# Optimization experiments

Measured on AMD Instinct MI355X. Metric: run time of the kernel, lower is better.

## Reference

```python
import jax, jax.numpy as jnp
import numpy as np
import math

LEVEL_SHAPES = [(100, 152), (50, 76), (25, 38), (13, 19)]
BS, E, NH, NL, NP = 2, 256, 8, 4, 4


def _grid_init_bias(num_heads, num_levels, num_points):
    # faithful to MultiScaleDeformableAttention.init_weights sampling_offsets bias
    thetas = jnp.arange(num_heads, dtype=jnp.float32) * (2.0 * math.pi / num_heads)
    grid = jnp.stack([jnp.cos(thetas), jnp.sin(thetas)], -1)  # [H,2]
    grid = grid / jnp.max(jnp.abs(grid), axis=-1, keepdims=True)
    grid = jnp.tile(grid[:, None, None, :], (1, num_levels, num_points, 1))  # [H,L,P,2]
    scale = jnp.arange(1, num_points + 1, dtype=jnp.float32)[None, None, :, None]
    return (grid * scale).reshape(-1)


def setup_inputs() -> dict:
    key = jax.random.key(0)
    ks = jax.random.split(key, 10)
    nv = sum(h * w for h, w in LEVEL_SHAPES)  # 20197
    nq = nv
    query = jax.random.normal(ks[0], (BS, nq, E), dtype=jnp.float32)
    value = jax.random.normal(ks[1], (BS, nv, E), dtype=jnp.float32)
    reference_points = jax.random.uniform(ks[2], (BS, nq, NL, 2), dtype=jnp.float32)
    spatial_shapes = jnp.array(LEVEL_SHAPES, dtype=jnp.int32)
    sizes = [h * w for h, w in LEVEL_SHAPES]
    level_start_index = jnp.array(np.cumsum([0] + sizes)[:-1], dtype=jnp.int32)
    s = 1.0 / math.sqrt(E)
    # Linear params stored as [in, out]; y = x @ W + b
    Wv = jax.random.normal(ks[3], (E, E), dtype=jnp.float32) * s
    bv = jnp.zeros((E,), jnp.float32)
    Wso = jax.random.normal(ks[4], (E, NH * NL * NP * 2), dtype=jnp.float32) * 0.01
    bso = _grid_init_bias(NH, NL, NP)
    Waw = jax.random.normal(ks[5], (E, NH * NL * NP), dtype=jnp.float32) * 0.01
    baw = jnp.zeros((NH * NL * NP,), jnp.float32)
    Wo = jax.random.normal(ks[6], (E, E), dtype=jnp.float32) * s
    bo = jnp.zeros((E,), jnp.float32)
    return dict(query=query, value=value, reference_points=reference_points,
                spatial_shapes=spatial_shapes, level_start_index=level_start_index,
                Wv=Wv, bv=bv, Wso=Wso, bso=bso, Waw=Waw, baw=baw, Wo=Wo, bo=bo)


def _bilinear_sample(vl, loc, h, w):
    # vl: [bs, nh, h*w, d]; loc: [bs, nq, nh, P, 2] normalized in [0,1]
    # matches F.grid_sample(mode='bilinear', padding_mode='zeros', align_corners=False)
    bs, nh, _, d = vl.shape
    nq, P = loc.shape[1], loc.shape[3]
    x = loc[..., 0] * w - 0.5
    y = loc[..., 1] * h - 0.5
    x0 = jnp.floor(x).astype(jnp.int32); x1 = x0 + 1
    y0 = jnp.floor(y).astype(jnp.int32); y1 = y0 + 1
    wx1 = x - x0; wx0 = 1.0 - wx1
    wy1 = y - y0; wy0 = 1.0 - wy1

    def gather(ix, iy):
        valid = ((ix >= 0) & (ix < w) & (iy >= 0) & (iy < h)).astype(vl.dtype)
        idx = jnp.clip(iy, 0, h - 1) * w + jnp.clip(ix, 0, w - 1)  # [bs,nq,nh,P]
        idx = jnp.transpose(idx, (0, 2, 1, 3)).reshape(bs, nh, nq * P)
        g = jnp.take_along_axis(vl, idx[..., None], axis=2)  # [bs,nh,nq*P,d]
        g = g.reshape(bs, nh, nq, P, d).transpose(0, 2, 1, 3, 4)  # [bs,nq,nh,P,d]
        return g * valid[..., None]

    return (gather(x0, y0) * (wx0 * wy0)[..., None]
            + gather(x1, y0) * (wx1 * wy0)[..., None]
            + gather(x0, y1) * (wx0 * wy1)[..., None]
            + gather(x1, y1) * (wx1 * wy1)[..., None])


def reference(query, value, reference_points, spatial_shapes, level_start_index,
              Wv, bv, Wso, bso, Waw, baw, Wo, bo):
    bs, nq, e = query.shape
    nv = value.shape[1]
    nh, nl, npt = NH, NL, NP
    d = e // nh
    shapes = np.asarray(spatial_shapes)          # static level shapes
    starts = np.asarray(level_start_index)

    v = (value @ Wv + bv).reshape(bs, nv, nh, d).transpose(0, 2, 1, 3)  # [bs,nh,nv,d]
    so = (query @ Wso + bso).reshape(bs, nq, nh, nl, npt, 2)
    aw = jax.nn.softmax((query @ Waw + baw).reshape(bs, nq, nh, nl * npt), axis=-1)
    aw = aw.reshape(bs, nq, nh, nl, npt)

    # offset normalizer is (w, h) per level
    offset_norm = jnp.stack([spatial_shapes[:, 1], spatial_shapes[:, 0]], -1).astype(query.dtype)
    loc = reference_points[:, :, None, :, None, :] + so / offset_norm[None, None, None, :, None, :]

    out = jnp.zeros((bs, nq, nh, d), dtype=query.dtype)
    for l in range(nl):
        h, w = int(shapes[l, 0]), int(shapes[l, 1])
        s = int(starts[l])
        vl = v[:, :, s:s + h * w, :]                      # [bs,nh,h*w,d]
        sampled = _bilinear_sample(vl, loc[:, :, :, l], h, w)  # [bs,nq,nh,P,d]
        out = out + jnp.einsum('bqhpd,bqhp->bqhd', sampled, aw[:, :, :, l])

    out = out.reshape(bs, nq, e) @ Wo + bo
    return out + query  # identity residual (dropout in eval mode)
```

## Files before the change

kernel.cpp:

```cpp
#include <hip/hip_runtime.h>
#include <hip/hip_bf16.h>
#include <math.h>

constexpr int kBS = 2;
constexpr int kNQ = 20197;
constexpr int kNV = 20197;
constexpr int kM  = kBS * kNQ;
constexpr int kMT = 632;
constexpr int kMpad = kMT * 64;

__constant__ int cLH[4] = {100, 50, 25, 13};
__constant__ int cLW[4] = {152, 76, 38, 19};
__constant__ int cLS[4] = {0, 15200, 19000, 19950};

typedef __bf16 bf16x8 __attribute__((ext_vector_type(8)));
typedef float  f32x4  __attribute__((ext_vector_type(4)));

__device__ __forceinline__ unsigned short f2bf(float x) {
    unsigned u = __float_as_uint(x);
    return (unsigned short)((u + 0x7fffu + ((u >> 16) & 1u)) >> 16);
}
__device__ __forceinline__ unsigned pack2(float a, float b) {
    return (unsigned)f2bf(a) | ((unsigned)f2bf(b) << 16);
}
__device__ __forceinline__ float bflo(unsigned u) { return __uint_as_float(u << 16); }
__device__ __forceinline__ float bfhi(unsigned u) { return __uint_as_float(u & 0xffff0000u); }
__device__ __forceinline__ void gload_lds16(const void* g, void* s) {
    __builtin_amdgcn_global_load_lds(
        (const __attribute__((address_space(1))) void*)g,
        (__attribute__((address_space(3))) void*)s, 16, 0, 0);
}

__global__ __launch_bounds__(256) void prep_w(
    const float* __restrict__ Wv, const float* __restrict__ Wso,
    const float* __restrict__ Waw, const float* __restrict__ Wo,
    const float* __restrict__ bso, const float* __restrict__ baw,
    unsigned short* __restrict__ WvT, unsigned short* __restrict__ WsoawT,
    unsigned short* __restrict__ WoT, float* __restrict__ bias384)
{
    int k = blockIdx.x * 256 + threadIdx.x;
    if (k < 65536) { WvT[k] = f2bf(Wv[(k & 255) * 256 + (k >> 8)]); return; }
    k -= 65536;
    if (k < 98304) {
        int n = k >> 8, kk = k & 255;
        WsoawT[k] = f2bf(n < 256 ? Wso[kk * 256 + n] : Waw[kk * 128 + (n - 256)]);
        return;
    }
    k -= 98304;
    if (k < 65536) { WoT[k] = f2bf(Wo[(k & 255) * 256 + (k >> 8)]); return; }
    k -= 65536;
    if (k < 384) bias384[k] = (k < 256) ? bso[k] : baw[k - 256];
}

template<int AFP32, int CFP32>
__device__ __forceinline__ void gemm_core(
    const void* __restrict__ Av, const __hip_bfloat16* __restrict__ BT,
    const float* __restrict__ bias, const float* __restrict__ res,
    int N, int NT, void* __restrict__ Cv, int m0)
{
    __shared__ __hip_bfloat16 As[64 * 264];
    __shared__ __hip_bfloat16 Bs[2][128 * 32];

    const int t = threadIdx.x;
    const int wave = t >> 6, lane = t & 63;
    const int quad = lane >> 4, l16 = lane & 15;
    const int mw = (wave & 1) * 32, nw = (wave >> 1) * 64;

    auto issueB = [&](int nti, int kc, int buf) {
        #pragma unroll
        for (int j = 0; j < 2; ++j) {
            int off = j * 4096 + t * 16;
            int row = off >> 6, kb = off & 63;
            gload_lds16((const char*)BT + (size_t)(nti * 128 + row) * 512 + kc * 64 + kb,
                        (char*)&Bs[buf][0] + off);
        }
    };

    issueB(0, 0, 0);

    if (AFP32) {
        const float* af = (const float*)Av;
        #pragma unroll
        for (int p = 0; p < 16; ++p) {
            int idx = p * 256 + t;
            int row = idx >> 6, col4 = idx & 63;
            float4 f = make_float4(0.f, 0.f, 0.f, 0.f);
            if (m0 + row < kM)
                f = *(const float4*)(af + (size_t)(m0 + row) * 256 + col4 * 4);
            uint2 u = make_uint2(pack2(f.x, f.y), pack2(f.z, f.w));
            *(uint2*)(void*)&As[row * 264 + col4 * 4] = u;
        }
    } else {
        const unsigned short* ab = (const unsigned short*)Av;
        #pragma unroll
        for (int p = 0; p < 8; ++p) {
            int idx = p * 256 + t;
            int row = idx >> 5, ch = idx & 31;
            uint4 u = *(const uint4*)(ab + (size_t)(m0 + row) * 256 + ch * 8);
            *(uint4*)(void*)&As[row * 264 + ch * 8] = u;
        }
    }

    for (int nti = 0; nti < NT; ++nti) {
        f32x4 acc[2][4] = {};
        for (int kc = 0; kc < 8; ++kc) {
            __syncthreads();
            if (kc < 7)             issueB(nti, kc + 1, (kc + 1) & 1);
            else if (nti + 1 < NT)  issueB(nti + 1, 0, 0);
            bf16x8 afr[2], bfr[4];
            #pragma unroll
            for (int mt = 0; mt < 2; ++mt)
                afr[mt] = *(const bf16x8*)(const void*)
                    &As[(mw + mt * 16 + l16) * 264 + kc * 32 + quad * 8];
            #pragma unroll
            for (int nt = 0; nt < 4; ++nt)
                bfr[nt] = *(const bf16x8*)(const void*)
                    &Bs[kc & 1][(nw + nt * 16 + l16) * 32 + quad * 8];
            #pragma unroll
            for (int mt = 0; mt < 2; ++mt)
                #pragma unroll
                for (int nt = 0; nt < 4; ++nt)
                    acc[mt][nt] = __builtin_amdgcn_mfma_f32_16x16x32_bf16(
                        afr[mt], bfr[nt], acc[mt][nt], 0, 0, 0);
        }
        const int n0g = nti * 128;
        #pragma unroll
        for (int nt = 0; nt < 4; ++nt) {
            int col = n0g + nw + nt * 16 + l16;
            float bvv = bias[col];
            #pragma unroll
            for (int mt = 0; mt < 2; ++mt) {
                #pragma unroll
                for (int i = 0; i < 4; ++i) {
                    int row = m0 + mw + mt * 16 + quad * 4 + i;
                    if (row < kM) {
                        float val = acc[mt][nt][i] + bvv;
                        if (CFP32)
                            ((float*)Cv)[(size_t)row * N + col] =
                                val + res[(size_t)row * N + col];
                        else
                            ((unsigned short*)Cv)[(size_t)row * N + col] = f2bf(val);
                    }
                }
            }
        }
    }
}

__global__ __launch_bounds__(256, 3) void gemm_dual(
    const float* __restrict__ value, const __hip_bfloat16* __restrict__ WvT,
    const float* __restrict__ bv, unsigned short* __restrict__ v_b,
    const float* __restrict__ query, const __hip_bfloat16* __restrict__ WsoawT,
    const float* __restrict__ b384, unsigned short* __restrict__ soaw)
{
    const int m0 = blockIdx.y * 64;
    const float* A; const __hip_bfloat16* BT; const float* bias;
    unsigned short* C; int N, NT;
    if (blockIdx.x == 0) { A = value; BT = WvT;    bias = bv;   C = v_b;  N = 256; NT = 2; }
    else                 { A = query; BT = WsoawT; bias = b384; C = soaw; N = 384; NT = 3; }
    gemm_core<1, 0>(A, BT, bias, nullptr, N, NT, C, m0);
}

__global__ __launch_bounds__(256, 3) void gemm_final(
    const unsigned short* __restrict__ mid_b, const __hip_bfloat16* __restrict__ WoT,
    const float* __restrict__ bo, const float* __restrict__ query,
    float* __restrict__ out)
{
    gemm_core<0, 1>(mid_b, WoT, bo, query, 256, 2, out, blockIdx.y * 64);
}

__global__ __launch_bounds__(128) void msda_sample(
    const __hip_bfloat16* __restrict__ v,
    const __hip_bfloat16* __restrict__ soaw,
    const float* __restrict__ rp,
    __hip_bfloat16* __restrict__ mid)
{
    const int bq = blockIdx.x;
    const int b  = bq >= kNQ;
    const int t  = threadIdx.x;

    __shared__ int   sOff[128 * 5];
    __shared__ float sW[128 * 5];

    {
        const int h = t >> 4, lp = t & 15, l = lp >> 2;
        unsigned sopk = *(const unsigned*)(const void*)(soaw + (size_t)bq * 384 + 2 * t);
        float logit = bflo((unsigned)*(const unsigned short*)(const void*)
                           (soaw + (size_t)bq * 384 + 256 + t));
        float2 rr = *(const float2*)(rp + (size_t)bq * 8 + l * 2);
        float sx = bflo(sopk), sy = bfhi(sopk);

        float mx = logit;
        #pragma unroll
        for (int s = 8; s >= 1; s >>= 1) mx = fmaxf(mx, __shfl_xor(mx, s, 16));
        float e = __expf(logit - mx);
        float sum = e;
        #pragma unroll
        for (int s = 8; s >= 1; s >>= 1) sum += __shfl_xor(sum, s, 16);
        float w = e / sum;

        const int ww = cLW[l], hh = cLH[l];
        const float fw = (float)ww, fh = (float)hh;
        float x = rr.x * fw + sx - 0.5f;
        float y = rr.y * fh + sy - 0.5f;
        float xf = floorf(x), yf = floorf(y);
        int x0 = (int)xf, y0 = (int)yf;
        float wx1 = x - xf, wx0 = 1.f - wx1;
        float wy1 = y - yf, wy0 = 1.f - wy1;
        bool vx0 = (x0 >= 0) & (x0 < ww);
        bool vx1 = (x0 >= -1) & (x0 + 1 < ww);
        bool vy0 = (y0 >= 0) & (y0 < hh);
        bool vy1 = (y0 >= -1) & (y0 + 1 < hh);
        int cx0 = min(max(x0, 0), ww - 1);
        int cx1 = min(max(x0 + 1, 0), ww - 1);
        int cy0 = min(max(y0, 0), hh - 1);
        int cy1 = min(max(y0 + 1, 0), hh - 1);
        const int base = cLS[l] * 256 + h * 32;
        sOff[t * 5 + 0] = base + (cy0 * ww + cx0) * 256;
        sOff[t * 5 + 1] = base + (cy0 * ww + cx1) * 256;
        sOff[t * 5 + 2] = base + (cy1 * ww + cx0) * 256;
        sOff[t * 5 + 3] = base + (cy1 * ww + cx1) * 256;
        sW[t * 5 + 0] = (vx0 & vy0) ? w * wx0 * wy0 : 0.f;
        sW[t * 5 + 1] = (vx1 & vy0) ? w * wx1 * wy0 : 0.f;
        sW[t * 5 + 2] = (vx0 & vy1) ? w * wx0 * wy1 : 0.f;
        sW[t * 5 + 3] = (vx1 & vy1) ? w * wx1 * wy1 : 0.f;
    }
    __syncthreads();

    const int h = t >> 4, c = (t & 15) * 2;
    const __hip_bfloat16* vb = v + (size_t)b * kNV * 256 + c;
    float accx = 0.f, accy = 0.f;
    const int p0 = h * 16;
    #pragma unroll 4
    for (int pp = 0; pp < 16; ++pp) {
        const int idx = (p0 + pp) * 5;
        #pragma unroll
        for (int k2 = 0; k2 < 4; ++k2) {
            float wgt = sW[idx + k2];
            int   off = sOff[idx + k2];
            unsigned u = *(const unsigned*)(const void*)(vb + off);
            accx += wgt * bflo(u);
            accy += wgt * bfhi(u);
        }
    }
    *(unsigned*)(void*)(mid + (size_t)bq * 256 + h * 32 + c) = pack2(accx, accy);
}

extern "C" void kernel_launch(void* const* d_in, const int* in_sizes, int n_in,
                              void* d_out, int out_size, void* d_ws, size_t ws_size,
                              hipStream_t stream)
{
    const float* query = (const float*)d_in[0];
    const float* value = (const float*)d_in[1];
    const float* rp    = (const float*)d_in[2];
    const float* Wv  = (const float*)d_in[5];
    const float* bv  = (const float*)d_in[6];
    const float* Wso = (const float*)d_in[7];
    const float* bso = (const float*)d_in[8];
    const float* Waw = (const float*)d_in[9];
    const float* baw = (const float*)d_in[10];
    const float* Wo  = (const float*)d_in[11];
    const float* bo  = (const float*)d_in[12];

    unsigned short* v_b = (unsigned short*)d_out;

    char* p = (char*)d_ws;
    __hip_bfloat16* soaw  = (__hip_bfloat16*)p;  p += (size_t)kM * 384 * 2;
    unsigned short* mid_b = (unsigned short*)p;  p += (size_t)kMpad * 256 * 2;
    unsigned short* WvT    = (unsigned short*)p; p += 256 * 256 * 2;
    unsigned short* WsoawT = (unsigned short*)p; p += 384 * 256 * 2;
    unsigned short* WoT    = (unsigned short*)p; p += 256 * 256 * 2;
    float* bias384         = (float*)p;

    hipLaunchKernelGGL(prep_w, dim3(898), dim3(256), 0, stream,
                       Wv, Wso, Waw, Wo, bso, baw, WvT, WsoawT, WoT, bias384);

    hipLaunchKernelGGL(gemm_dual, dim3(2, kMT), dim3(256), 0, stream,
                       value, (const __hip_bfloat16*)WvT, bv, v_b,
                       query, (const __hip_bfloat16*)WsoawT, bias384,
                       (unsigned short*)soaw);

    hipLaunchKernelGGL(msda_sample, dim3(kM), dim3(128), 0, stream,
                       (const __hip_bfloat16*)v_b, soaw, rp, (__hip_bfloat16*)mid_b);

    hipLaunchKernelGGL(gemm_final, dim3(1, kMT), dim3(256), 0, stream,
                       mid_b, (const __hip_bfloat16*)WoT, bo, query, (float*)d_out);
}
```

Before: 299.9 us.

## Deepen GEMM B pipeline, swizzle LDS, pack sampler offsets/weights, coalesce weight prep

The GEMM core moves to a 4-buffer B-tile pipeline with three chunks in flight, using explicit vmcnt waits and raw barriers, and replaces padded LDS rows with XOR swizzles for both A and B. The bf16 A path now loads straight to LDS, and the fp32 A path issues all global loads before converting. The sampler stores offset and weight pairs as one int2 in LDS, uses byte offsets and packed f32x2 FMA, and unrolls deeper. Weight prep now reads coalesced. The changes aim to hide load latency and cut bank conflicts and address arithmetic, at the cost of lower occupancy (launch bounds 3→2) and fragile hand-written waitcnt logic.

```diff
diff --git a/kernel.cpp b/kernel.cpp
--- a/kernel.cpp
+++ b/kernel.cpp
@@ -15,6 +15,7 @@
 
 typedef __bf16 bf16x8 __attribute__((ext_vector_type(8)));
 typedef float  f32x4  __attribute__((ext_vector_type(4)));
+typedef float  f32x2  __attribute__((ext_vector_type(2)));
 
 __device__ __forceinline__ unsigned short f2bf(float x) {
     unsigned u = __float_as_uint(x);
@@ -30,6 +31,11 @@
         (const __attribute__((address_space(1))) void*)g,
         (__attribute__((address_space(3))) void*)s, 16, 0, 0);
 }
+__device__ __forceinline__ void vmwait(int n) {
+    if (n == 0)      asm volatile("s_waitcnt vmcnt(0)" ::: "memory");
+    else if (n == 2) asm volatile("s_waitcnt vmcnt(2)" ::: "memory");
+    else             asm volatile("s_waitcnt vmcnt(4)" ::: "memory");
+}
 
 __global__ __launch_bounds__(256) void prep_w(
     const float* __restrict__ Wv, const float* __restrict__ Wso,
@@ -39,15 +45,13 @@
     unsigned short* __restrict__ WoT, float* __restrict__ bias384)
 {
     int k = blockIdx.x * 256 + threadIdx.x;
-    if (k < 65536) { WvT[k] = f2bf(Wv[(k & 255) * 256 + (k >> 8)]); return; }
+    if (k < 65536) { int kk = k >> 8, n = k & 255; WvT[n * 256 + kk] = f2bf(Wv[k]); return; }
     k -= 65536;
-    if (k < 98304) {
-        int n = k >> 8, kk = k & 255;
-        WsoawT[k] = f2bf(n < 256 ? Wso[kk * 256 + n] : Waw[kk * 128 + (n - 256)]);
-        return;
-    }
-    k -= 98304;
-    if (k < 65536) { WoT[k] = f2bf(Wo[(k & 255) * 256 + (k >> 8)]); return; }
+    if (k < 65536) { int kk = k >> 8, n = k & 255; WsoawT[n * 256 + kk] = f2bf(Wso[k]); return; }
+    k -= 65536;
+    if (k < 32768) { int kk = k >> 7, n = k & 127; WsoawT[(256 + n) * 256 + kk] = f2bf(Waw[k]); return; }
+    k -= 32768;
+    if (k < 65536) { int kk = k >> 8, n = k & 255; WoT[n * 256 + kk] = f2bf(Wo[k]); return; }
     k -= 65536;
     if (k < 384) bias384[k] = (k < 256) ? bso[k] : baw[k - 256];
 }
@@ -58,64 +62,88 @@
     const float* __restrict__ bias, const float* __restrict__ res,
     int N, int NT, void* __restrict__ Cv, int m0)
 {
-    __shared__ __hip_bfloat16 As[64 * 264];
-    __shared__ __hip_bfloat16 Bs[2][128 * 32];
+    __shared__ __hip_bfloat16 As[64 * 256];
+    __shared__ __hip_bfloat16 Bs[4][128 * 32];
 
     const int t = threadIdx.x;
     const int wave = t >> 6, lane = t & 63;
     const int quad = lane >> 4, l16 = lane & 15;
     const int mw = (wave & 1) * 32, nw = (wave >> 1) * 64;
-
-    auto issueB = [&](int nti, int kc, int buf) {
+    const int NCH = NT * 8;
+
+    auto issueB = [&](int g) {
+        const int nti = g >> 3, kc = g & 7, buf = g & 3;
         #pragma unroll
         for (int j = 0; j < 2; ++j) {
-            int off = j * 4096 + t * 16;
-            int row = off >> 6, kb = off & 63;
-            gload_lds16((const char*)BT + (size_t)(nti * 128 + row) * 512 + kc * 64 + kb,
-                        (char*)&Bs[buf][0] + off);
+            int s = j * 256 + t;
+            int row = s >> 2;
+            int ql = (s & 3) ^ ((row >> 1) & 3);
+            gload_lds16((const char*)BT + (size_t)(nti * 128 + row) * 512
+                            + kc * 64 + ql * 16,
+                        (char*)&Bs[buf][0] + s * 16);
         }
     };
-
-    issueB(0, 0, 0);
 
     if (AFP32) {
         const float* af = (const float*)Av;
+        float4 fr[16];
         #pragma unroll
         for (int p = 0; p < 16; ++p) {
             int idx = p * 256 + t;
             int row = idx >> 6, col4 = idx & 63;
-            float4 f = make_float4(0.f, 0.f, 0.f, 0.f);
+            fr[p] = make_float4(0.f, 0.f, 0.f, 0.f);
             if (m0 + row < kM)
-                f = *(const float4*)(af + (size_t)(m0 + row) * 256 + col4 * 4);
-            uint2 u = make_uint2(pack2(f.x, f.y), pack2(f.z, f.w));
-            *(uint2*)(void*)&As[row * 264 + col4 * 4] = u;
-        }
+                fr[p] = *(const float4*)(af + (size_t)(m0 + row) * 256 + col4 * 4);
+        }
+        issueB(0); issueB(1); issueB(2);
+        #pragma unroll
+        for (int p = 0; p < 16; ++p) {
+            int idx = p * 256 + t;
+            int row = idx >> 6, col4 = idx & 63;
+            int ps = (col4 >> 1) ^ (row & 7);
+            uint2 u = make_uint2(pack2(fr[p].x, fr[p].y), pack2(fr[p].z, fr[p].w));
+            *(uint2*)(void*)((char*)As + row * 512 + ps * 16 + (col4 & 1) * 8) = u;
+        }
+        asm volatile("s_waitcnt lgkmcnt(0)" ::: "memory");
     } else {
         const unsigned short* ab = (const unsigned short*)Av;
         #pragma unroll
         for (int p = 0; p < 8; ++p) {
-            int idx = p * 256 + t;
-            int row = idx >> 5, ch = idx & 31;
-            uint4 u = *(const uint4*)(ab + (size_t)(m0 + row) * 256 + ch * 8);
-            *(uint4*)(void*)&As[row * 264 + ch * 8] = u;
-        }
+            int s = p * 256 + t;
+            int row = s >> 5;
+            int slog = (s & 31) ^ (row & 7);
+            gload_lds16(ab + (size_t)(m0 + row) * 256 + slog * 8,
+                        (char*)As + s * 16);
+        }
+        issueB(0); issueB(1); issueB(2);
     }
 
     for (int nti = 0; nti < NT; ++nti) {
         f32x4 acc[2][4] = {};
+        #pragma unroll
         for (int kc = 0; kc < 8; ++kc) {
-            __syncthreads();
-            if (kc < 7)             issueB(nti, kc + 1, (kc + 1) & 1);
-            else if (nti + 1 < NT)  issueB(nti + 1, 0, 0);
+            const int g = nti * 8 + kc;
+            const int left = NCH - 1 - g;
+            vmwait(left >= 2 ? 4 : 2 * left);
+            asm volatile("s_barrier" ::: "memory");
+            if (g + 3 < NCH) issueB(g + 3);
+
+            const int buf = g & 3;
             bf16x8 afr[2], bfr[4];
             #pragma unroll
-            for (int mt = 0; mt < 2; ++mt)
+            for (int mt = 0; mt < 2; ++mt) {
+                int row = mw + mt * 16 + l16;
+                int ps = (kc * 4 + quad) ^ (row & 7);
                 afr[mt] = *(const bf16x8*)(const void*)
-                    &As[(mw + mt * 16 + l16) * 264 + kc * 32 + quad * 8];
+                    ((const char*)As + row * 512 + ps * 16);
+            }
             #pragma unroll
-            for (int nt = 0; nt < 4; ++nt)
+            for (int nt = 0; nt < 4; ++nt) {
+                int r = nw + nt * 16 + l16;
+                int qp = quad ^ ((r >> 1) & 3);
                 bfr[nt] = *(const bf16x8*)(const void*)
-                    &Bs[kc & 1][(nw + nt * 16 + l16) * 32 + quad * 8];
+                    ((const char*)&Bs[buf][0] + r * 64 + qp * 16);
+            }
             #pragma unroll
             for (int mt = 0; mt < 2; ++mt)
                 #pragma unroll
@@ -147,7 +175,7 @@
     }
 }
 
-__global__ __launch_bounds__(256, 3) void gemm_dual(
+__global__ __launch_bounds__(256, 2) void gemm_dual(
     const float* __restrict__ value, const __hip_bfloat16* __restrict__ WvT,
     const float* __restrict__ bv, unsigned short* __restrict__ v_b,
     const float* __restrict__ query, const __hip_bfloat16* __restrict__ WsoawT,
@@ -161,7 +189,7 @@
     gemm_core<1, 0>(A, BT, bias, nullptr, N, NT, C, m0);
 }
 
-__global__ __launch_bounds__(256, 3) void gemm_final(
+__global__ __launch_bounds__(256, 2) void gemm_final(
     const unsigned short* __restrict__ mid_b, const __hip_bfloat16* __restrict__ WoT,
     const float* __restrict__ bo, const float* __restrict__ query,
     float* __restrict__ out)
@@ -179,8 +207,7 @@
     const int b  = bq >= kNQ;
     const int t  = threadIdx.x;
 
-    __shared__ int   sOff[128 * 5];
-    __shared__ float sW[128 * 5];
+    __shared__ int2 sP[128 * 5];
 
     {
         const int h = t >> 4, lp = t & 15, l = lp >> 2;
@@ -215,35 +242,37 @@
         int cx1 = min(max(x0 + 1, 0), ww - 1);
         int cy0 = min(max(y0, 0), hh - 1);
         int cy1 = min(max(y0 + 1, 0), hh - 1);
-        const int base = cLS[l] * 256 + h * 32;
-        sOff[t * 5 + 0] = base + (cy0 * ww + cx0) * 256;
-        sOff[t * 5 + 1] = base + (cy0 * ww + cx1) * 256;
-        sOff[t * 5 + 2] = base + (cy1 * ww + cx0) * 256;
-        sOff[t * 5 + 3] = base + (cy1 * ww + cx1) * 256;
-        sW[t * 5 + 0] = (vx0 & vy0) ? w * wx0 * wy0 : 0.f;
-        sW[t * 5 + 1] = (vx1 & vy0) ? w * wx1 * wy0 : 0.f;
-        sW[t * 5 + 2] = (vx0 & vy1) ? w * wx0 * wy1 : 0.f;
-        sW[t * 5 + 3] = (vx1 & vy1) ? w * wx1 * wy1 : 0.f;
+        const int base2 = cLS[l] * 512 + h * 64;
+        sP[t * 5 + 0] = make_int2(base2 + (cy0 * ww + cx0) * 512,
+                                  __float_as_int((vx0 & vy0) ? w * wx0 * wy0 : 0.f));
+        sP[t * 5 + 1] = make_int2(base2 + (cy0 * ww + cx1) * 512,
+                                  __float_as_int((vx1 & vy0) ? w * wx1 * wy0 : 0.f));
+        sP[t * 5 + 2] = make_int2(base2 + (cy1 * ww + cx0) * 512,
+                                  __float_as_int((vx0 & vy1) ? w * wx0 * wy1 : 0.f));
+        sP[t * 5 + 3] = make_int2(base2 + (cy1 * ww + cx1) * 512,
+                                  __float_as_int((vx1 & vy1) ? w * wx1 * wy1 : 0.f));
     }
     __syncthreads();
 
     const int h = t >> 4, c = (t & 15) * 2;
-    const __hip_bfloat16* vb = v + (size_t)b * kNV * 256 + c;
-    float accx = 0.f, accy = 0.f;
+    const char* vb = (const char*)v + (size_t)b * ((size_t)kNV * 512);
+    const unsigned cb = (unsigned)(c * 2);
+    f32x2 acc = {0.f, 0.f};
     const int p0 = h * 16;
-    #pragma unroll 4
+    #pragma unroll 8
     for (int pp = 0; pp < 16; ++pp) {
         const int idx = (p0 + pp) * 5;
         #pragma unroll
         for (int k2 = 0; k2 < 4; ++k2) {
-            float wgt = sW[idx + k2];
-            int   off = sOff[idx + k2];
-            unsigned u = *(const unsigned*)(const void*)(vb + off);
-            accx += wgt * bflo(u);
-            accy += wgt * bfhi(u);
+            int2 pw = sP[idx + k2];
+            float wgt = __int_as_float(pw.y);
+            unsigned u = *(const unsigned*)(const void*)(vb + ((unsigned)pw.x + cb));
+            f32x2 xy; xy.x = bflo(u); xy.y = bfhi(u);
+            f32x2 w2; w2.x = wgt; w2.y = wgt;
+            acc = xy * w2 + acc;
         }
     }
-    *(unsigned*)(void*)(mid + (size_t)bq * 256 + h * 32 + c) = pack2(accx, accy);
+    *(unsigned*)(void*)(mid + (size_t)bq * 256 + h * 32 + c) = pack2(acc.x, acc.y);
 }
 
 extern "C" void kernel_launch(void* const* d_in, const int* in_sizes, int n_in,
```

Measured after the change: 326.0 us. 1.09x slower.
